# Kernel tuning notes

Measured on AMD Instinct MI355X. Metric: run time of the kernel, lower is better.

## Reference

```python
import jax, jax.numpy as jnp
import numpy as np

CHANNELS = [4096, 4096, 4096, 4096]
SPARSITY = 0.9  # fraction of weight entries zeroed (sten.random_mask_sparsify frac)
BATCH = 4096


def _sparse_weight(key, out_f, in_f, frac):
    kw, km = jax.random.split(key)
    w = jax.random.normal(kw, (out_f, in_f), dtype=jnp.float32)
    keep = jax.random.uniform(km, (out_f, in_f)) >= frac  # keep ~(1-frac) entries
    return jnp.where(keep, w, 0.0)


def setup_inputs() -> dict:
    key = jax.random.key(0)
    ks = jax.random.split(key, 7)
    x = jax.random.normal(ks[0], (BATCH, CHANNELS[0]), dtype=jnp.float32)
    W1 = _sparse_weight(ks[1], CHANNELS[1], CHANNELS[0], SPARSITY)
    b1 = jax.random.uniform(ks[2], (CHANNELS[1],), dtype=jnp.float32)
    W2 = _sparse_weight(ks[3], CHANNELS[2], CHANNELS[1], SPARSITY)
    b2 = jax.random.uniform(ks[4], (CHANNELS[2],), dtype=jnp.float32)
    W3 = _sparse_weight(ks[5], CHANNELS[3], CHANNELS[2], SPARSITY)
    b3 = jax.random.uniform(ks[6], (CHANNELS[3],), dtype=jnp.float32)
    return {"x": x, "W1": W1, "b1": b1, "W2": W2, "b2": b2, "W3": W3, "b3": b3}


def reference(x, W1, b1, W2, b2, W3, b3):
    # Sequential: Linear -> ReLU -> Linear -> ReLU -> Linear
    # F.linear(x, W, b) == x @ W.T + b; weights already carry the sparsity mask.
    h = x @ W1.T + b1
    h = jax.nn.relu(h)
    h = h @ W2.T + b2
    h = jax.nn.relu(h)
    return h @ W3.T + b3
```

## Files before the change

### kernel.cpp

```cpp
#include <hip/hip_runtime.h>
#include <cstdint>


#define MATN 4096
#define NT (MATN / 64)

typedef _Float16 half8 __attribute__((ext_vector_type(8)));
typedef float f32x4 __attribute__((ext_vector_type(4)));

__device__ __forceinline__ void glds16(const void* g, void* l) {
    __builtin_amdgcn_global_load_lds(
        (const __attribute__((address_space(1))) char*)(uintptr_t)g,
        (__attribute__((address_space(3))) char*)(uintptr_t)l,
        16, 0, 0);
}

__device__ __forceinline__ void cvt_body(const float* __restrict__ in,
                                         _Float16* __restrict__ out, int n8) {
    for (int g = blockIdx.x * 256 + threadIdx.x; g < n8; g += gridDim.x * 256) {
        size_t i = (size_t)g * 8;
        float4 a = *(const float4*)(in + i);
        float4 b = *(const float4*)(in + i + 4);
        half8 o;
        o[0] = (_Float16)a.x; o[1] = (_Float16)a.y;
        o[2] = (_Float16)a.z; o[3] = (_Float16)a.w;
        o[4] = (_Float16)b.x; o[5] = (_Float16)b.y;
        o[6] = (_Float16)b.z; o[7] = (_Float16)b.w;
        *(half8*)(out + i) = o;
    }
}

__global__ __launch_bounds__(256)
void cvt_f16(const float* __restrict__ in, _Float16* __restrict__ out, int n8) {
    cvt_body(in, out, n8);
}

__global__ __launch_bounds__(256)
void cvt_f16_2(const float* __restrict__ i0, _Float16* __restrict__ o0,
               const float* __restrict__ i1, _Float16* __restrict__ o1, int n8) {
    cvt_body(blockIdx.y ? i1 : i0, blockIdx.y ? o1 : o0, n8);
}

__global__ __launch_bounds__(256)
void cvt_f16_4(const float* __restrict__ i0, _Float16* __restrict__ o0,
               const float* __restrict__ i1, _Float16* __restrict__ o1,
               const float* __restrict__ i2, _Float16* __restrict__ o2,
               const float* __restrict__ i3, _Float16* __restrict__ o3, int n8) {
    const float* in;
    _Float16* out;
    switch (blockIdx.y) {
        case 0: in = i0; out = o0; break;
        case 1: in = i1; out = o1; break;
        case 2: in = i2; out = o2; break;
        default: in = i3; out = o3; break;
    }
    cvt_body(in, out, n8);
}

#define MFMA_(d, x, y) d = __builtin_amdgcn_mfma_f32_16x16x32_f16(x, y, d, 0, 0, 0)

template <bool RELU, typename OutT>
__global__ __launch_bounds__(512, 2)
void gemm_bt(const _Float16* __restrict__ A, const _Float16* __restrict__ B,
             const float* __restrict__ bias, OutT* __restrict__ C) {
    __shared__ _Float16 lds[2][4][128 * 64];

    const int tid  = threadIdx.x;
    const int lane = tid & 63;
    const int w    = tid >> 6;
    const int wm   = w >> 2;
    const int wn   = w & 3;
    const int l16  = lane & 15;
    const int kq   = lane >> 4;

    const int bid   = blockIdx.y * 16 + blockIdx.x;
    const int sbid  = (bid & 7) * 32 + (bid >> 3);
    const int tileM = (sbid >> 4) * 256;
    const int tileN = (sbid & 15) * 256;

    char* const ldsb = (char*)lds;

    const int rowStage = ((tid >> 7) & 3) * 16 + l16;
    const int colStage = (w & 1) * 32 + kq * 8;
    const _Float16* const aS = A + (size_t)(tileM + rowStage) * MATN + colStage;
    const _Float16* const bS = B + (size_t)(tileN + rowStage) * MATN + colStage;

#define STAGE_(Tt, reg, half, src)                                             \
    do {                                                                       \
        if ((Tt) < NT) {                                                       \
            const _Float16* g_ =                                               \
                (src) + (size_t)((half) * 128) * MATN + (Tt) * 64;             \
            char* l_ = ldsb + (((Tt) & 1) * 4 + (reg)) * 16384 + w * 1024;     \
            glds16(g_, l_);                                                    \
            glds16(g_ + (size_t)64 * MATN, l_ + 8192);                         \
        }                                                                      \
    } while (0)
#define STAGE_A(Tt, mh) STAGE_(Tt, (mh) * 3, mh, aS)
#define STAGE_B(Tt, nh) STAGE_(Tt, 1 + (nh), nh, bS)

    half8 aP[4], aQ[4], bP[4], bQ[4];
    f32x4 acc[8][4] = {};

    STAGE_A(0, 0);
    STAGE_B(0, 0);
    STAGE_B(0, 1);
    STAGE_A(0, 1);
    STAGE_B(1, 1);
    asm volatile("s_waitcnt vmcnt(2)" ::: "memory");
    __builtin_amdgcn_s_barrier();

#pragma unroll 2
    for (int T = 0; T < NT; ++T) {
        const char* Ard = ldsb + (T & 1) * 65536 + wm * 3 * 16384 + lane * 16;
        const char* Brd = ldsb + (T & 1) * 65536 + (1 + (wn >> 1)) * 16384 +
                          (wn & 1) * 8192 + lane * 16;

#pragma unroll
        for (int mi = 0; mi < 4; ++mi)
            aP[mi] = *(const half8*)(Ard + mi * 2048);
#pragma unroll
        for (int ni = 0; ni < 4; ++ni)
            bP[ni] = *(const half8*)(Brd + ni * 2048);
#pragma unroll
        for (int mi = 0; mi < 4; ++mi)
            aQ[mi] = *(const half8*)(Ard + 8192 + mi * 2048);
        STAGE_A(T + 1, 0);
        __builtin_amdgcn_s_barrier();
        asm volatile("s_waitcnt lgkmcnt(0)" ::: "memory");
        __builtin_amdgcn_sched_barrier(0);
        __builtin_amdgcn_s_setprio(1);
#pragma unroll
        for (int mi = 0; mi < 4; ++mi)
#pragma unroll
            for (int ni = 0; ni < 4; ++ni)
                MFMA_(acc[mi][ni], aP[mi], bP[ni]);
        __builtin_amdgcn_s_setprio(0);
        __builtin_amdgcn_s_barrier();

#pragma unroll
        for (int mi = 0; mi < 4; ++mi)
            aP[mi] = *(const half8*)(Ard + 8192 + mi * 2048 + 1024);
#pragma unroll
        for (int ni = 0; ni < 4; ++ni)
            bQ[ni] = *(const half8*)(Brd + ni * 2048 + 1024);
        STAGE_A(T + 1, 1);
        __builtin_amdgcn_s_barrier();
        asm volatile("s_waitcnt lgkmcnt(8)" ::: "memory");
        __builtin_amdgcn_sched_barrier(0);
        __builtin_amdgcn_s_setprio(1);
#pragma unroll
        for (int mi = 0; mi < 4; ++mi)
#pragma unroll
            for (int ni = 0; ni < 4; ++ni)
                MFMA_(acc[4 + mi][ni], aQ[mi], bP[ni]);
        __builtin_amdgcn_s_setprio(0);
        __builtin_amdgcn_s_barrier();

#pragma unroll
        for (int mi = 0; mi < 4; ++mi)
            aQ[mi] = *(const half8*)(Ard + mi * 2048 + 1024);
        STAGE_B(T + 1, 0);
        __builtin_amdgcn_s_barrier();
        asm volatile("s_waitcnt lgkmcnt(4)" ::: "memory");
        __builtin_amdgcn_sched_barrier(0);
        __builtin_amdgcn_s_setprio(1);
#pragma unroll
        for (int mi = 0; mi < 4; ++mi)
#pragma unroll
            for (int ni = 0; ni < 4; ++ni)
                MFMA_(acc[4 + mi][ni], aP[mi], bQ[ni]);
        __builtin_amdgcn_s_setprio(0);
        __builtin_amdgcn_s_barrier();

        STAGE_B(T + 2, 1);
        __builtin_amdgcn_s_barrier();
        asm volatile("s_waitcnt lgkmcnt(0)" ::: "memory");
        __builtin_amdgcn_sched_barrier(0);
        __builtin_amdgcn_s_setprio(1);
#pragma unroll
        for (int mi = 0; mi < 4; ++mi)
#pragma unroll
            for (int ni = 0; ni < 4; ++ni)
                MFMA_(acc[mi][ni], aQ[mi], bQ[ni]);
        __builtin_amdgcn_s_setprio(0);
        if (T < NT - 2)
            asm volatile("s_waitcnt vmcnt(2)" ::: "memory");
        else
            asm volatile("s_waitcnt vmcnt(0)" ::: "memory");
        __builtin_amdgcn_s_barrier();
    }
#undef STAGE_A
#undef STAGE_B
#undef STAGE_

#pragma unroll
    for (int ni = 0; ni < 4; ++ni) {
        const int gn = tileN + wn * 64 + ni * 16 + l16;
        const float bv = bias[gn];
#pragma unroll
        for (int mi = 0; mi < 8; ++mi) {
            const int gm = tileM + wm * 128 + mi * 16 + kq * 4;
#pragma unroll
            for (int r = 0; r < 4; ++r) {
                float v = acc[mi][ni][r] + bv;
                if (RELU) v = v > 0.f ? v : 0.f;
                C[(size_t)(gm + r) * MATN + gn] = (OutT)v;
            }
        }
    }
}

extern "C" void kernel_launch(void* const* d_in, const int* in_sizes, int n_in,
                              void* d_out, int out_size, void* d_ws, size_t ws_size,
                              hipStream_t stream) {
    const float* x  = (const float*)d_in[0];
    const float* W1 = (const float*)d_in[1];
    const float* b1 = (const float*)d_in[2];
    const float* W2 = (const float*)d_in[3];
    const float* b2 = (const float*)d_in[4];
    const float* W3 = (const float*)d_in[5];
    const float* b3 = (const float*)d_in[6];
    float* out = (float*)d_out;

    const size_t MAT = (size_t)MATN * MATN;
    const size_t HB  = MAT * 2;
    const int n8 = (int)(MAT / 8);
    dim3 ggrid(MATN / 256, MATN / 256);

    if (ws_size >= HB * 5) {
        _Float16* xb = (_Float16*)d_ws;
        _Float16* w1 = (_Float16*)((char*)d_ws + HB);
        _Float16* w2 = (_Float16*)((char*)d_ws + HB * 2);
        _Float16* w3 = (_Float16*)((char*)d_ws + HB * 3);
        _Float16* h1 = (_Float16*)((char*)d_ws + HB * 4);
        _Float16* h2 = xb;

        cvt_f16_4<<<dim3(2048, 4), 256, 0, stream>>>(x, xb, W1, w1, W2, w2,
                                                     W3, w3, n8);
        gemm_bt<true, _Float16><<<ggrid, 512, 0, stream>>>(xb, w1, b1, h1);
        gemm_bt<true, _Float16><<<ggrid, 512, 0, stream>>>(h1, w2, b2, h2);
        gemm_bt<false, float><<<ggrid, 512, 0, stream>>>(h2, w3, b3, out);
    } else {
        _Float16* xb = (_Float16*)d_ws;
        _Float16* wb = (_Float16*)((char*)d_ws + HB);
        _Float16* h1 = (_Float16*)((char*)d_ws + HB * 2);
        _Float16* h2 = xb;

        cvt_f16_2<<<dim3(2048, 2), 256, 0, stream>>>(x, xb, W1, wb, n8);
        gemm_bt<true, _Float16><<<ggrid, 512, 0, stream>>>(xb, wb, b1, h1);
        cvt_f16<<<2048, 256, 0, stream>>>(W2, wb, n8);
        gemm_bt<true, _Float16><<<ggrid, 512, 0, stream>>>(h1, wb, b2, h2);
        cvt_f16<<<2048, 256, 0, stream>>>(W3, wb, n8);
        gemm_bt<false, float><<<ggrid, 512, 0, stream>>>(h2, wb, b3, out);
    }
}
```

Baseline: 661.1 us.

## Pre-tile fp16 operands into MFMA-blocked layout for contiguous LDS staging

The conversion kernels now write fp16 copies of x and the weights in a blocked layout (16-row by 64-column tiles, 2 KB chunks). Each wave's global-to-LDS load is therefore a fully contiguous 1 KB segment instead of strided row fragments. The intermediate activations h1 and h2 are written back in the same blocked layout so the next GEMM can consume them directly. The main loop is also restructured into four phases with a different register reuse pattern and deeper vmcnt waits. The costs are scattered 2-byte stores in the epilogue and strided reads in the conversion kernels.

```diff
diff --git a/kernel.cpp b/kernel.cpp
--- a/kernel.cpp
+++ b/kernel.cpp
@@ -15,37 +15,44 @@
         16, 0, 0);
 }
 
-__device__ __forceinline__ void cvt_body(const float* __restrict__ in,
-                                         _Float16* __restrict__ out, int n8) {
-    for (int g = blockIdx.x * 256 + threadIdx.x; g < n8; g += gridDim.x * 256) {
-        size_t i = (size_t)g * 8;
-        float4 a = *(const float4*)(in + i);
-        float4 b = *(const float4*)(in + i + 4);
+__device__ __forceinline__ void cvtblk_body(const float* __restrict__ in,
+                                            _Float16* __restrict__ out, int n16) {
+    for (int g = blockIdx.x * 256 + threadIdx.x; g < n16; g += gridDim.x * 256) {
+        const int r16 = g & 15;
+        const int kq  = (g >> 4) & 3;
+        const int ks  = (g >> 6) & 1;
+        const int T   = (g >> 7) & 63;
+        const int R   = g >> 13;
+        const size_t row = (size_t)R * 16 + r16;
+        const int    col = T * 64 + ks * 32 + kq * 8;
+        const float* p = in + row * MATN + col;
+        float4 a = *(const float4*)p;
+        float4 b = *(const float4*)(p + 4);
         half8 o;
         o[0] = (_Float16)a.x; o[1] = (_Float16)a.y;
         o[2] = (_Float16)a.z; o[3] = (_Float16)a.w;
         o[4] = (_Float16)b.x; o[5] = (_Float16)b.y;
         o[6] = (_Float16)b.z; o[7] = (_Float16)b.w;
-        *(half8*)(out + i) = o;
+        *(half8*)(out + (size_t)g * 8) = o;
     }
 }
 
 __global__ __launch_bounds__(256)
-void cvt_f16(const float* __restrict__ in, _Float16* __restrict__ out, int n8) {
-    cvt_body(in, out, n8);
+void cvt_blk(const float* __restrict__ in, _Float16* __restrict__ out, int n16) {
+    cvtblk_body(in, out, n16);
 }
 
 __global__ __launch_bounds__(256)
-void cvt_f16_2(const float* __restrict__ i0, _Float16* __restrict__ o0,
-               const float* __restrict__ i1, _Float16* __restrict__ o1, int n8) {
-    cvt_body(blockIdx.y ? i1 : i0, blockIdx.y ? o1 : o0, n8);
+void cvt_blk2(const float* __restrict__ i0, _Float16* __restrict__ o0,
+              const float* __restrict__ i1, _Float16* __restrict__ o1, int n16) {
+    cvtblk_body(blockIdx.y ? i1 : i0, blockIdx.y ? o1 : o0, n16);
 }
 
 __global__ __launch_bounds__(256)
-void cvt_f16_4(const float* __restrict__ i0, _Float16* __restrict__ o0,
-               const float* __restrict__ i1, _Float16* __restrict__ o1,
-               const float* __restrict__ i2, _Float16* __restrict__ o2,
-               const float* __restrict__ i3, _Float16* __restrict__ o3, int n8) {
+void cvt_blk4(const float* __restrict__ i0, _Float16* __restrict__ o0,
+              const float* __restrict__ i1, _Float16* __restrict__ o1,
+              const float* __restrict__ i2, _Float16* __restrict__ o2,
+              const float* __restrict__ i3, _Float16* __restrict__ o3, int n16) {
     const float* in;
     _Float16* out;
     switch (blockIdx.y) {
@@ -54,15 +61,15 @@
         case 2: in = i2; out = o2; break;
         default: in = i3; out = o3; break;
     }
-    cvt_body(in, out, n8);
+    cvtblk_body(in, out, n16);
 }
 
 #define MFMA_(d, x, y) d = __builtin_amdgcn_mfma_f32_16x16x32_f16(x, y, d, 0, 0, 0)
 
-template <bool RELU, typename OutT>
+template <bool RELU, bool OBLK, typename OutT>
 __global__ __launch_bounds__(512, 2)
-void gemm_bt(const _Float16* __restrict__ A, const _Float16* __restrict__ B,
-             const float* __restrict__ bias, OutT* __restrict__ C) {
+void gemm_blk(const _Float16* __restrict__ A, const _Float16* __restrict__ B,
+              const float* __restrict__ bias, OutT* __restrict__ C) {
     __shared__ _Float16 lds[2][4][128 * 64];
 
     const int tid  = threadIdx.x;
@@ -80,131 +87,150 @@
 
     char* const ldsb = (char*)lds;
 
-    const int rowStage = ((tid >> 7) & 3) * 16 + l16;
-    const int colStage = (w & 1) * 32 + kq * 8;
-    const _Float16* const aS = A + (size_t)(tileM + rowStage) * MATN + colStage;
-    const _Float16* const bS = B + (size_t)(tileN + rowStage) * MATN + colStage;
-
-#define STAGE_(Tt, reg, half, src)                                             \
+    const int lb = lane * 16;
+    const char* const aSrc =
+        (const char*)A + ((size_t)((tileM >> 4) + w) * 131072) + lb;
+    const char* const bSrc =
+        (const char*)B + ((size_t)((tileN >> 4) + w) * 131072) + lb;
+    const int wj = w * 2048;
+
+#define SA(Tt, h, j)                                                           \
     do {                                                                       \
-        if ((Tt) < NT) {                                                       \
-            const _Float16* g_ =                                               \
-                (src) + (size_t)((half) * 128) * MATN + (Tt) * 64;             \
-            char* l_ = ldsb + (((Tt) & 1) * 4 + (reg)) * 16384 + w * 1024;     \
-            glds16(g_, l_);                                                    \
-            glds16(g_ + (size_t)64 * MATN, l_ + 8192);                         \
-        }                                                                      \
+        if ((Tt) < NT)                                                         \
+            glds16(aSrc + (size_t)(h)*1048576 + (size_t)(Tt)*2048 + (j)*1024,  \
+                   ldsb + ((Tt)&1) * 65536 + (h)*49152 + wj + (j)*1024);       \
     } while (0)
-#define STAGE_A(Tt, mh) STAGE_(Tt, (mh) * 3, mh, aS)
-#define STAGE_B(Tt, nh) STAGE_(Tt, 1 + (nh), nh, bS)
-
-    half8 aP[4], aQ[4], bP[4], bQ[4];
+#define SB(Tt, h, j)                                                           \
+    do {                                                                       \
+        if ((Tt) < NT)                                                         \
+            glds16(bSrc + (size_t)(h)*1048576 + (size_t)(Tt)*2048 + (j)*1024,  \
+                   ldsb + ((Tt)&1) * 65536 + 16384 + (h)*16384 + wj +          \
+                       (j)*1024);                                              \
+    } while (0)
+
+    half8 aP[4], bP[4], bQ[4];
     f32x4 acc[8][4] = {};
 
-    STAGE_A(0, 0);
-    STAGE_B(0, 0);
-    STAGE_B(0, 1);
-    STAGE_A(0, 1);
-    STAGE_B(1, 1);
-    asm volatile("s_waitcnt vmcnt(2)" ::: "memory");
+    SA(0, 0, 0); SA(0, 1, 0);
+    SB(0, 0, 0); SB(0, 1, 0);
+    SA(0, 0, 1); SA(0, 1, 1);
+    SB(0, 0, 1); SB(0, 1, 1);
+    asm volatile("s_waitcnt vmcnt(4)" ::: "memory");
     __builtin_amdgcn_s_barrier();
 
-#pragma unroll 2
     for (int T = 0; T < NT; ++T) {
-        const char* Ard = ldsb + (T & 1) * 65536 + wm * 3 * 16384 + lane * 16;
-        const char* Brd = ldsb + (T & 1) * 65536 + (1 + (wn >> 1)) * 16384 +
-                          (wn & 1) * 8192 + lane * 16;
-
-#pragma unroll
-        for (int mi = 0; mi < 4; ++mi)
-            aP[mi] = *(const half8*)(Ard + mi * 2048);
-#pragma unroll
-        for (int ni = 0; ni < 4; ++ni)
-            bP[ni] = *(const half8*)(Brd + ni * 2048);
-#pragma unroll
-        for (int mi = 0; mi < 4; ++mi)
-            aQ[mi] = *(const half8*)(Ard + 8192 + mi * 2048);
-        STAGE_A(T + 1, 0);
-        __builtin_amdgcn_s_barrier();
-        asm volatile("s_waitcnt lgkmcnt(0)" ::: "memory");
-        __builtin_amdgcn_sched_barrier(0);
-        __builtin_amdgcn_s_setprio(1);
-#pragma unroll
-        for (int mi = 0; mi < 4; ++mi)
-#pragma unroll
-            for (int ni = 0; ni < 4; ++ni)
-                MFMA_(acc[mi][ni], aP[mi], bP[ni]);
-        __builtin_amdgcn_s_setprio(0);
-        __builtin_amdgcn_s_barrier();
-
-#pragma unroll
-        for (int mi = 0; mi < 4; ++mi)
-            aP[mi] = *(const half8*)(Ard + 8192 + mi * 2048 + 1024);
-#pragma unroll
-        for (int ni = 0; ni < 4; ++ni)
-            bQ[ni] = *(const half8*)(Brd + ni * 2048 + 1024);
-        STAGE_A(T + 1, 1);
-        __builtin_amdgcn_s_barrier();
-        asm volatile("s_waitcnt lgkmcnt(8)" ::: "memory");
-        __builtin_amdgcn_sched_barrier(0);
-        __builtin_amdgcn_s_setprio(1);
-#pragma unroll
-        for (int mi = 0; mi < 4; ++mi)
-#pragma unroll
-            for (int ni = 0; ni < 4; ++ni)
-                MFMA_(acc[4 + mi][ni], aQ[mi], bP[ni]);
-        __builtin_amdgcn_s_setprio(0);
-        __builtin_amdgcn_s_barrier();
-
-#pragma unroll
-        for (int mi = 0; mi < 4; ++mi)
-            aQ[mi] = *(const half8*)(Ard + mi * 2048 + 1024);
-        STAGE_B(T + 1, 0);
-        __builtin_amdgcn_s_barrier();
-        asm volatile("s_waitcnt lgkmcnt(4)" ::: "memory");
-        __builtin_amdgcn_sched_barrier(0);
-        __builtin_amdgcn_s_setprio(1);
-#pragma unroll
-        for (int mi = 0; mi < 4; ++mi)
-#pragma unroll
-            for (int ni = 0; ni < 4; ++ni)
-                MFMA_(acc[4 + mi][ni], aP[mi], bQ[ni]);
-        __builtin_amdgcn_s_setprio(0);
-        __builtin_amdgcn_s_barrier();
-
-        STAGE_B(T + 2, 1);
-        __builtin_amdgcn_s_barrier();
-        asm volatile("s_waitcnt lgkmcnt(0)" ::: "memory");
-        __builtin_amdgcn_sched_barrier(0);
-        __builtin_amdgcn_s_setprio(1);
-#pragma unroll
-        for (int mi = 0; mi < 4; ++mi)
-#pragma unroll
-            for (int ni = 0; ni < 4; ++ni)
-                MFMA_(acc[mi][ni], aQ[mi], bQ[ni]);
-        __builtin_amdgcn_s_setprio(0);
-        if (T < NT - 2)
-            asm volatile("s_waitcnt vmcnt(2)" ::: "memory");
+        const char* bufb = ldsb + (T & 1) * 65536;
+        const char* Ard  = bufb + wm * 49152 + lb;
+        const char* Brd  = bufb + 16384 + (wn >> 1) * 16384 + (wn & 1) * 8192 + lb;
+
+#pragma unroll
+        for (int i = 0; i < 4; ++i) aP[i] = *(const half8*)(Ard + i * 2048);
+#pragma unroll
+        for (int n = 0; n < 4; ++n) bP[n] = *(const half8*)(Brd + n * 2048);
+        SA(T + 1, 0, 0); SA(T + 1, 1, 0);
+        __builtin_amdgcn_s_barrier();
+        asm volatile("s_waitcnt lgkmcnt(0)" ::: "memory");
+        __builtin_amdgcn_sched_barrier(0);
+        __builtin_amdgcn_s_setprio(1);
+#pragma unroll
+        for (int i = 0; i < 4; ++i)
+#pragma unroll
+            for (int n = 0; n < 4; ++n) MFMA_(acc[i][n], aP[i], bP[n]);
+        __builtin_amdgcn_s_setprio(0);
+        __builtin_amdgcn_s_barrier();
+
+#pragma unroll
+        for (int i = 0; i < 4; ++i)
+            aP[i] = *(const half8*)(Ard + 8192 + i * 2048);
+        SB(T + 1, 0, 0); SB(T + 1, 1, 0);
+        __builtin_amdgcn_s_barrier();
+        asm volatile("s_waitcnt lgkmcnt(0)" ::: "memory");
+        __builtin_amdgcn_sched_barrier(0);
+        __builtin_amdgcn_s_setprio(1);
+#pragma unroll
+        for (int i = 0; i < 4; ++i)
+#pragma unroll
+            for (int n = 0; n < 4; ++n) MFMA_(acc[4 + i][n], aP[i], bP[n]);
+        __builtin_amdgcn_s_setprio(0);
+        if (T < NT - 1)
+            asm volatile("s_waitcnt vmcnt(4)" ::: "memory");
         else
             asm volatile("s_waitcnt vmcnt(0)" ::: "memory");
         __builtin_amdgcn_s_barrier();
-    }
-#undef STAGE_A
-#undef STAGE_B
-#undef STAGE_
-
-#pragma unroll
-    for (int ni = 0; ni < 4; ++ni) {
-        const int gn = tileN + wn * 64 + ni * 16 + l16;
-        const float bv = bias[gn];
-#pragma unroll
-        for (int mi = 0; mi < 8; ++mi) {
-            const int gm = tileM + wm * 128 + mi * 16 + kq * 4;
-#pragma unroll
-            for (int r = 0; r < 4; ++r) {
-                float v = acc[mi][ni][r] + bv;
-                if (RELU) v = v > 0.f ? v : 0.f;
-                C[(size_t)(gm + r) * MATN + gn] = (OutT)v;
+
+#pragma unroll
+        for (int i = 0; i < 4; ++i)
+            aP[i] = *(const half8*)(Ard + 9216 + i * 2048);
+#pragma unroll
+        for (int n = 0; n < 4; ++n)
+            bQ[n] = *(const half8*)(Brd + 1024 + n * 2048);
+        SA(T + 1, 0, 1); SA(T + 1, 1, 1);
+        __builtin_amdgcn_s_barrier();
+        asm volatile("s_waitcnt lgkmcnt(0)" ::: "memory");
+        __builtin_amdgcn_sched_barrier(0);
+        __builtin_amdgcn_s_setprio(1);
+#pragma unroll
+        for (int i = 0; i < 4; ++i)
+#pragma unroll
+            for (int n = 0; n < 4; ++n) MFMA_(acc[4 + i][n], aP[i], bQ[n]);
+        __builtin_amdgcn_s_setprio(0);
+        __builtin_amdgcn_s_barrier();
+
+#pragma unroll
+        for (int i = 0; i < 4; ++i)
+            aP[i] = *(const half8*)(Ard + 1024 + i * 2048);
+        SB(T + 1, 0, 1); SB(T + 1, 1, 1);
+        __builtin_amdgcn_s_barrier();
+        asm volatile("s_waitcnt lgkmcnt(0)" ::: "memory");
+        __builtin_amdgcn_sched_barrier(0);
+        __builtin_amdgcn_s_setprio(1);
+#pragma unroll
+        for (int i = 0; i < 4; ++i)
+#pragma unroll
+            for (int n = 0; n < 4; ++n) MFMA_(acc[i][n], aP[i], bQ[n]);
+        __builtin_amdgcn_s_setprio(0);
+        asm volatile("s_waitcnt vmcnt(4)" ::: "memory");
+        __builtin_amdgcn_s_barrier();
+    }
+#undef SA
+#undef SB
+
+    if (OBLK) {
+        char* const Cb = (char*)C;
+        const int tN0 = tileN >> 6;
+#pragma unroll
+        for (int ni = 0; ni < 4; ++ni) {
+            const int q  = ni * 16 + l16;
+            const float bv = bias[tileN + wn * 64 + q];
+            const size_t colOff = (size_t)(((tN0 + wn) * 2 + ((q >> 5) & 1))) * 1024 +
+                                  ((q >> 3) & 3) * 256 + (q & 7) * 2;
+#pragma unroll
+            for (int mi = 0; mi < 8; ++mi) {
+                const size_t Roff =
+                    (size_t)((tileM >> 4) + wm * 8 + mi) * 131072;
+#pragma unroll
+                for (int r = 0; r < 4; ++r) {
+                    float v = acc[mi][ni][r] + bv;
+                    if (RELU) v = v > 0.f ? v : 0.f;
+                    *(_Float16*)(Cb + Roff + colOff + (kq * 4 + r) * 16) =
+                        (_Float16)v;
+                }
+            }
+        }
+    } else {
+#pragma unroll
+        for (int ni = 0; ni < 4; ++ni) {
+            const int gn = tileN + wn * 64 + ni * 16 + l16;
+            const float bv = bias[gn];
+#pragma unroll
+            for (int mi = 0; mi < 8; ++mi) {
+                const int gm = tileM + wm * 128 + mi * 16 + kq * 4;
+#pragma unroll
+                for (int r = 0; r < 4; ++r) {
+                    float v = acc[mi][ni][r] + bv;
+                    if (RELU) v = v > 0.f ? v : 0.f;
+                    C[(size_t)(gm + r) * MATN + gn] = (OutT)v;
+                }
             }
         }
     }
@@ -224,7 +250,7 @@
 
     const size_t MAT = (size_t)MATN * MATN;
     const size_t HB  = MAT * 2;
-    const int n8 = (int)(MAT / 8);
+    const int n16 = (int)(MAT / 8);
     dim3 ggrid(MATN / 256, MATN / 256);
 
     if (ws_size >= HB * 5) {
@@ -235,22 +261,22 @@
         _Float16* h1 = (_Float16*)((char*)d_ws + HB * 4);
         _Float16* h2 = xb;
 
-        cvt_f16_4<<<dim3(2048, 4), 256, 0, stream>>>(x, xb, W1, w1, W2, w2,
-                                                     W3, w3, n8);
-        gemm_bt<true, _Float16><<<ggrid, 512, 0, stream>>>(xb, w1, b1, h1);
-        gemm_bt<true, _Float16><<<ggrid, 512, 0, stream>>>(h1, w2, b2, h2);
-        gemm_bt<false, float><<<ggrid, 512, 0, stream>>>(h2, w3, b3, out);
+        cvt_blk4<<<dim3(8192, 4), 256, 0, stream>>>(x, xb, W1, w1, W2, w2,
+                                                    W3, w3, n16);
+        gemm_blk<true, true, _Float16><<<ggrid, 512, 0, stream>>>(xb, w1, b1, h1);
+        gemm_blk<true, true, _Float16><<<ggrid, 512, 0, stream>>>(h1, w2, b2, h2);
+        gemm_blk<false, false, float><<<ggrid, 512, 0, stream>>>(h2, w3, b3, out);
     } else {
         _Float16* xb = (_Float16*)d_ws;
         _Float16* wb = (_Float16*)((char*)d_ws + HB);
         _Float16* h1 = (_Float16*)((char*)d_ws + HB * 2);
         _Float16* h2 = xb;
 
-        cvt_f16_2<<<dim3(2048, 2), 256, 0, stream>>>(x, xb, W1, wb, n8);
-        gemm_bt<true, _Float16><<<ggrid, 512, 0, stream>>>(xb, wb, b1, h1);
-        cvt_f16<<<2048, 256, 0, stream>>>(W2, wb, n8);
-        gemm_bt<true, _Float16><<<ggrid, 512, 0, stream>>>(h1, wb, b2, h2);
-        cvt_f16<<<2048, 256, 0, stream>>>(W3, wb, n8);
-        gemm_bt<false, float><<<ggrid, 512, 0, stream>>>(h2, wb, b3, out);
-    }
-}
+        cvt_blk2<<<dim3(8192, 2), 256, 0, stream>>>(x, xb, W1, wb, n16);
+        gemm_blk<true, true, _Float16><<<ggrid, 512, 0, stream>>>(xb, wb, b1, h1);
+        cvt_blk<<<8192, 256, 0, stream>>>(W2, wb, n16);
+        gemm_blk<true, true, _Float16><<<ggrid, 512, 0, stream>>>(h1, wb, b2, h2);
+        cvt_blk<<<8192, 256, 0, stream>>>(W3, wb, n16);
+        gemm_blk<false, false, float><<<ggrid, 512, 0, stream>>>(h2, wb, b3, out);
+    }
+}
```

Measured after the change: 577.9 us. 1.14x faster.
